# Kernel tuning notes

Hardware: AMD Instinct MI355X
Metric: run time of the kernel (lower is better)

## Reference

```python
import jax, jax.numpy as jnp
import numpy as np

CTX = 768   # ctx_len in the original module
C = 768     # n_embd
B = 16
T = 768
K_EPS = 1e-8


def setup_inputs() -> dict:
    key = jax.random.key(0)
    ks = jax.random.split(key, 10)
    scale = 1.0 / np.sqrt(C)
    x = jax.random.normal(ks[0], (B, T, C), jnp.float32)
    time_decay = jax.random.normal(ks[1], (C, 1), jnp.float32) * 0.1
    time_first = jnp.full((C, 1), np.log(0.3), jnp.float32)
    time_mix_k = jax.random.uniform(ks[2], (1, 1, C), jnp.float32)
    time_mix_v = jax.random.uniform(ks[3], (1, 1, C), jnp.float32)
    time_mix_r = jax.random.uniform(ks[4], (1, 1, C), jnp.float32)
    Wk = jax.random.normal(ks[5], (C, C), jnp.float32) * scale
    Wv = jax.random.normal(ks[6], (C, C), jnp.float32) * scale
    Wr = jax.random.normal(ks[7], (C, C), jnp.float32) * scale
    Wo = jax.random.normal(ks[8], (C, C), jnp.float32) * scale
    return {"x": x, "time_decay": time_decay, "time_first": time_first,
            "time_mix_k": time_mix_k, "time_mix_v": time_mix_v, "time_mix_r": time_mix_r,
            "Wk": Wk, "Wv": Wv, "Wr": Wr, "Wo": Wo}


def reference(x, time_decay, time_first, time_mix_k, time_mix_v, time_mix_r, Wk, Wv, Wr, Wo):
    Bb, Tt, Cc = x.shape
    # time_shift: xx[t] = x[t-1], xx[0] = 0
    xx = jnp.pad(x, ((0, 0), (1, 0), (0, 0)))[:, :Tt]
    xk = x * time_mix_k + xx * (1.0 - time_mix_k)
    xv = x * time_mix_v + xx * (1.0 - time_mix_v)
    xr = x * time_mix_r + xx * (1.0 - time_mix_r)
    # projections (nn.Linear, no bias: y = x @ W.T); k, v laid out [B, C, T]
    k = jnp.einsum('btc,oc->bot', xk, Wk)
    v = jnp.einsum('btc,oc->bot', xv, Wv)
    r = jnp.einsum('btc,oc->bto', xr, Wr)
    k = jnp.exp(jnp.minimum(k, 60.0))
    kv = k * v
    # decay kernel: time_w = cat([exp(time_decay)*time_curve, time_first]); w = exp(time_w)[:, -T:]
    curve = (jnp.arange(CTX - 1) - (CTX - 2)).astype(x.dtype)  # [-(CTX-2) .. 0]
    tw = jnp.concatenate([jnp.exp(time_decay) * curve[None, :], time_first], axis=-1)  # [C, CTX]
    w = jnp.exp(tw)[:, -Tt:]            # [C, T]
    kern = w[:, None, :]                # [C, 1, T] depthwise kernel

    def causal_conv(z):  # z: [B, C, T] -> [B, C, T], left-padded cross-correlation
        return jax.lax.conv_general_dilated(
            z, kern, window_strides=(1,), padding=[(Tt - 1, 0)],
            feature_group_count=Cc, dimension_numbers=('NCH', 'OIH', 'NCH'))

    wkv = causal_conv(kv)
    wk = causal_conv(k) + K_EPS
    rwkv = jax.nn.sigmoid(r) * jnp.transpose(wkv / wk, (0, 2, 1))  # [B, T, C]
    return jnp.einsum('btc,oc->bto', rwkv, Wo)
```

## Files before the change

kernel.cpp:

```cpp
#include <hip/hip_runtime.h>
#include <math.h>

#define Mq 12288
#define Nq 768
#define Kq 768
#define Tq 768
#define Bq 16
#define Cq 768
#define BK 64
#define BM 128

typedef __bf16 bf16x8 __attribute__((ext_vector_type(8)));
typedef __bf16 bf16x4 __attribute__((ext_vector_type(4)));
typedef __bf16 bf16x2 __attribute__((ext_vector_type(2)));
typedef float  floatx4 __attribute__((ext_vector_type(4)));

#define GLD_LDS16(g, l) __builtin_amdgcn_global_load_lds(                      \
    (const __attribute__((address_space(1))) unsigned int*)(g),                \
    (__attribute__((address_space(3))) unsigned int*)(l), 16, 0, 0)

__global__ __launch_bounds__(256)
void prep_kernel(const float* __restrict__ x,
                 const float* __restrict__ mk, const float* __restrict__ mv,
                 const float* __restrict__ mr,
                 const float* __restrict__ Wk, const float* __restrict__ Wv,
                 const float* __restrict__ Wr, const float* __restrict__ Wo,
                 __bf16* __restrict__ xk, __bf16* __restrict__ xv,
                 __bf16* __restrict__ xr, __bf16* __restrict__ wp)
{
    const int bid = blockIdx.x;
    if (bid < 9216) {
        const int i  = bid * 256 + threadIdx.x;
        const int c4 = i % (Cq / 4);
        const int m  = i / (Cq / 4);
        const int t  = m % Tq;
        const int c0 = c4 * 4;

        const float4 xc = *(const float4*)(x + (size_t)m * Cq + c0);
        float4 xp = make_float4(0.f, 0.f, 0.f, 0.f);
        if (t > 0) xp = *(const float4*)(x + (size_t)(m - 1) * Cq + c0);

        const float4 k4 = *(const float4*)(mk + c0);
        const float4 v4 = *(const float4*)(mv + c0);
        const float4 r4 = *(const float4*)(mr + c0);

        bf16x4 ok = { (__bf16)fmaf(k4.x, xc.x - xp.x, xp.x),
                      (__bf16)fmaf(k4.y, xc.y - xp.y, xp.y),
                      (__bf16)fmaf(k4.z, xc.z - xp.z, xp.z),
                      (__bf16)fmaf(k4.w, xc.w - xp.w, xp.w) };
        bf16x4 ov = { (__bf16)fmaf(v4.x, xc.x - xp.x, xp.x),
                      (__bf16)fmaf(v4.y, xc.y - xp.y, xp.y),
                      (__bf16)fmaf(v4.z, xc.z - xp.z, xp.z),
                      (__bf16)fmaf(v4.w, xc.w - xp.w, xp.w) };
        bf16x4 orr = { (__bf16)fmaf(r4.x, xc.x - xp.x, xp.x),
                       (__bf16)fmaf(r4.y, xc.y - xp.y, xp.y),
                       (__bf16)fmaf(r4.z, xc.z - xp.z, xp.z),
                       (__bf16)fmaf(r4.w, xc.w - xp.w, xp.w) };
        const size_t o = (size_t)m * Cq + c0;
        *(bf16x4*)(xk + o) = ok;
        *(bf16x4*)(xv + o) = ov;
        *(bf16x4*)(xr + o) = orr;
    } else {
        const int i   = (bid - 9216) * 256 + threadIdx.x;
        const int a   = i / 147456;
        const int off = (i - a * 147456) * 4;
        const float* s = (a == 0) ? Wk : (a == 1) ? Wv : (a == 2) ? Wr : Wo;
        const float4 v = *(const float4*)(s + off);
        bf16x4 r = { (__bf16)v.x, (__bf16)v.y, (__bf16)v.z, (__bf16)v.w };
        *(bf16x4*)(wp + (size_t)a * 589824 + off) = r;
    }
}

template<bool KVR>
__global__ __launch_bounds__(256, 3)
void mfma_gemm(const __bf16* __restrict__ A0, const __bf16* __restrict__ A1,
               const __bf16* __restrict__ A2,
               const __bf16* __restrict__ W,
               __bf16* __restrict__ OUTb, float* __restrict__ OUTf)
{
    __shared__ __bf16 As[BM * BK];
    __shared__ __bf16 Bs[128 * BK];

    const int STRIPS = KVR ? 18 : 6;

    const int i_    = blockIdx.x;
    const int xcd   = i_ & 7;
    const int j_    = i_ >> 3;
    const int strip = j_ % STRIPS;
    const int mt    = xcd * 12 + j_ / STRIPS;

    const int tid   = threadIdx.x;
    const int wave  = tid >> 6;
    const int lane  = tid & 63;
    const int m0    = mt * BM;
    const int matid = KVR ? strip / 6 : 0;
    const int n0    = KVR ? (strip % 6) * 128 : strip * 128;
    const int wn0   = strip * 128;

    const __bf16* A = KVR ? (matid == 0 ? A0 : matid == 1 ? A1 : A2) : A0;

    const int r8 = lane >> 3;
    const int sc = (lane & 7) ^ r8;
    const __bf16* gA[4];  __bf16* lA[4];
    const __bf16* gB[4];  __bf16* lB[4];
#pragma unroll
    for (int i = 0; i < 4; ++i) {
        const int row = (wave * 4 + i) * 8 + r8;
        gA[i] = A + (size_t)(m0 + row) * Kq + sc * 8;
        lA[i] = As + (wave * 4 + i) * 512;
        gB[i] = W + (size_t)(wn0 + row) * Kq + sc * 8;
        lB[i] = Bs + (wave * 4 + i) * 512;
    }

    const int wm   = wave & 1;
    const int wn   = wave >> 1;
    const int xRow = wm * 64 + (lane & 15);
    const int wRow = wn * 64 + (lane & 15);
    const int lk   = lane >> 4;

    floatx4 acc[4][4];
#pragma unroll
    for (int i = 0; i < 4; ++i)
#pragma unroll
        for (int j = 0; j < 4; ++j) acc[i][j] = (floatx4){0.f, 0.f, 0.f, 0.f};

    for (int kt = 0; kt < Kq / BK; ++kt) {
#pragma unroll
        for (int i = 0; i < 4; ++i) { GLD_LDS16(gA[i], lA[i]); gA[i] += BK; }
#pragma unroll
        for (int i = 0; i < 4; ++i) { GLD_LDS16(gB[i], lB[i]); gB[i] += BK; }
        __syncthreads();

#pragma unroll
        for (int kk = 0; kk < 2; ++kk) {
            bf16x8 wF[4], xF[4];
#pragma unroll
            for (int i = 0; i < 4; ++i) {
                const int r = wRow + i * 16;
                wF[i] = *(const bf16x8*)(Bs + r * BK +
                                         (((kk << 2) | lk) ^ (r & 7)) * 8);
            }
#pragma unroll
            for (int j = 0; j < 4; ++j) {
                const int r = xRow + j * 16;
                xF[j] = *(const bf16x8*)(As + r * BK +
                                         (((kk << 2) | lk) ^ (r & 7)) * 8);
            }
#pragma unroll
            for (int i = 0; i < 4; ++i)
#pragma unroll
                for (int j = 0; j < 4; ++j)
                    acc[i][j] = __builtin_amdgcn_mfma_f32_16x16x32_bf16(
                        wF[i], xF[j], acc[i][j], 0, 0, 0);
        }
        __syncthreads();
    }

#pragma unroll
    for (int j = 0; j < 4; ++j) {
        const int tok = m0 + wm * 64 + j * 16 + (lane & 15);
#pragma unroll
        for (int i = 0; i < 4; ++i) {
            const int ch = n0 + wn * 64 + i * 16 + (lane >> 4) * 4;
            if (KVR) {
                float v0 = acc[i][j][0], v1 = acc[i][j][1];
                float v2 = acc[i][j][2], v3 = acc[i][j][3];
                if (matid == 0) {
                    v0 = expf(fminf(v0, 60.f)); v1 = expf(fminf(v1, 60.f));
                    v2 = expf(fminf(v2, 60.f)); v3 = expf(fminf(v3, 60.f));
                } else if (matid == 2) {
                    v0 = __builtin_amdgcn_rcpf(1.f + expf(-v0));
                    v1 = __builtin_amdgcn_rcpf(1.f + expf(-v1));
                    v2 = __builtin_amdgcn_rcpf(1.f + expf(-v2));
                    v3 = __builtin_amdgcn_rcpf(1.f + expf(-v3));
                }
                bf16x4 o = { (__bf16)v0, (__bf16)v1, (__bf16)v2, (__bf16)v3 };
                *(bf16x4*)(OUTb + (size_t)matid * Mq * Nq +
                           (size_t)tok * Nq + ch) = o;
            } else {
                floatx4 o = acc[i][j];
                *(floatx4*)(OUTf + (size_t)tok * Nq + ch) = o;
            }
        }
    }
}

#define SEG 16
#define SLEN (Tq / SEG)

__global__ __launch_bounds__(1024)
void scan_kernel(const __bf16* __restrict__ kb, const __bf16* __restrict__ vb,
                 __bf16* rb,
                 const float* __restrict__ td, const float* __restrict__ tf)
{
    __shared__ float2 aS[SEG][64];
    __shared__ float2 bS[SEG][64];

    const int cx  = threadIdx.x;
    const int seg = threadIdx.y;
    const int c0  = blockIdx.x * 128 + cx * 2;
    const int b   = blockIdx.y;

    const float d0 = expf(td[c0]),     d1 = expf(td[c0 + 1]);
    const float w0 = expf(-d0),        w1 = expf(-d1);
    const float u0 = expf(tf[c0]),     u1 = expf(tf[c0 + 1]);

    const size_t base = ((size_t)b * Tq + seg * SLEN) * Cq + c0;

    float a0 = 0.f, a1 = 0.f, s0 = 0.f, s1 = 0.f;
#pragma unroll 4
    for (int t = 0; t < SLEN; ++t) {
        const size_t idx = base + (size_t)t * Cq;
        const bf16x2 k2 = *(const bf16x2*)(kb + idx);
        const bf16x2 v2 = *(const bf16x2*)(vb + idx);
        const float k0 = (float)k2[0], k1 = (float)k2[1];
        a0 = fmaf(w0, a0, k0 * (float)v2[0]);
        a1 = fmaf(w1, a1, k1 * (float)v2[1]);
        s0 = fmaf(w0, s0, k0);
        s1 = fmaf(w1, s1, k1);
    }
    aS[seg][cx] = make_float2(a0, a1);
    bS[seg][cx] = make_float2(s0, s1);
    __syncthreads();

    if (seg == 0) {
        const float W0 = expf(-d0 * (float)SLEN);
        const float W1 = expf(-d1 * (float)SLEN);
        float ia0 = 0.f, ia1 = 0.f, ib0 = 0.f, ib1 = 0.f;
#pragma unroll
        for (int s = 0; s < SEG; ++s) {
            const float2 ta = aS[s][cx];
            const float2 tb = bS[s][cx];
            aS[s][cx] = make_float2(ia0, ia1);
            bS[s][cx] = make_float2(ib0, ib1);
            ia0 = fmaf(W0, ia0, ta.x);  ia1 = fmaf(W1, ia1, ta.y);
            ib0 = fmaf(W0, ib0, tb.x);  ib1 = fmaf(W1, ib1, tb.y);
        }
    }
    __syncthreads();

    const float2 ain = aS[seg][cx];
    const float2 bin = bS[seg][cx];
    a0 = ain.x; a1 = ain.y; s0 = bin.x; s1 = bin.y;
#pragma unroll 2
    for (int t = 0; t < SLEN; ++t) {
        const size_t idx = base + (size_t)t * Cq;
        const bf16x2 k2 = *(const bf16x2*)(kb + idx);
        const bf16x2 v2 = *(const bf16x2*)(vb + idx);
        const bf16x2 r2 = *(const bf16x2*)(rb + idx);
        const float k0 = (float)k2[0], k1 = (float)k2[1];
        const float kv0 = k0 * (float)v2[0], kv1 = k1 * (float)v2[1];
        const float n0 = fmaf(u0, kv0, a0), n1 = fmaf(u1, kv1, a1);
        const float e0 = fmaf(u0, k0, s0) + 1e-8f;
        const float e1 = fmaf(u1, k1, s1) + 1e-8f;
        const float i0 = __builtin_amdgcn_rcpf(e0);
        const float i1 = __builtin_amdgcn_rcpf(e1);
        bf16x2 o = { (__bf16)((float)r2[0] * n0 * i0),
                     (__bf16)((float)r2[1] * n1 * i1) };
        *(bf16x2*)(rb + idx) = o;
        a0 = fmaf(w0, a0, kv0);  a1 = fmaf(w1, a1, kv1);
        s0 = fmaf(w0, s0, k0);   s1 = fmaf(w1, s1, k1);
    }
}

extern "C" void kernel_launch(void* const* d_in, const int* in_sizes, int n_in,
                              void* d_out, int out_size, void* d_ws, size_t ws_size,
                              hipStream_t stream)
{
    const float* x  = (const float*)d_in[0];
    const float* td = (const float*)d_in[1];
    const float* tf = (const float*)d_in[2];
    const float* mk = (const float*)d_in[3];
    const float* mv = (const float*)d_in[4];
    const float* mr = (const float*)d_in[5];
    const float* Wk = (const float*)d_in[6];
    const float* Wv = (const float*)d_in[7];
    const float* Wr = (const float*)d_in[8];
    const float* Wo = (const float*)d_in[9];

    const size_t MC = (size_t)Mq * Cq;

    __bf16* xk = (__bf16*)d_out;
    __bf16* xv = xk + MC;

    __bf16* xr   = (__bf16*)d_ws;
    __bf16* kbuf = xr + MC;
    __bf16* vbuf = kbuf + MC;
    __bf16* rbuf = vbuf + MC;
    __bf16* Wp   = rbuf + MC;
    __bf16* Wob  = Wp + 3 * 589824;

    prep_kernel<<<11520, 256, 0, stream>>>(x, mk, mv, mr, Wk, Wv, Wr, Wo,
                                           xk, xv, xr, Wp);

    mfma_gemm<true><<<18 * 96, 256, 0, stream>>>(
        xk, xv, xr, Wp, kbuf, nullptr);

    scan_kernel<<<dim3(Cq / 128, Bq), dim3(64, SEG), 0, stream>>>(
        kbuf, vbuf, rbuf, td, tf);

    mfma_gemm<false><<<6 * 96, 256, 0, stream>>>(
        rbuf, nullptr, nullptr, Wob, nullptr, (float*)d_out);
}
```

Before: 216.5 us.

## Fuse token-shift mixing into the KVR projection GEMM A-tile load

Removes the separate prep pass that wrote bf16 xk/xv/xr to memory. The KVR GEMM now loads fp32 x (current and previous row) directly, applies the time-mix, converts to bf16 and writes the A tile into LDS with regular stores. This saves the intermediate write and re-read of three activation tensors. The cost is that each of the six N-strips per matrix recomputes the mix and reads fp32 x twice, and the asynchronous global-to-LDS load for A is replaced by synchronous register loads with no overlap.

```diff
diff --git a/kernel.cpp b/kernel.cpp
--- a/kernel.cpp
+++ b/kernel.cpp
@@ -20,68 +20,30 @@
     (__attribute__((address_space(3))) unsigned int*)(l), 16, 0, 0)
 
 __global__ __launch_bounds__(256)
-void prep_kernel(const float* __restrict__ x,
-                 const float* __restrict__ mk, const float* __restrict__ mv,
-                 const float* __restrict__ mr,
-                 const float* __restrict__ Wk, const float* __restrict__ Wv,
-                 const float* __restrict__ Wr, const float* __restrict__ Wo,
-                 __bf16* __restrict__ xk, __bf16* __restrict__ xv,
-                 __bf16* __restrict__ xr, __bf16* __restrict__ wp)
-{
-    const int bid = blockIdx.x;
-    if (bid < 9216) {
-        const int i  = bid * 256 + threadIdx.x;
-        const int c4 = i % (Cq / 4);
-        const int m  = i / (Cq / 4);
-        const int t  = m % Tq;
-        const int c0 = c4 * 4;
-
-        const float4 xc = *(const float4*)(x + (size_t)m * Cq + c0);
-        float4 xp = make_float4(0.f, 0.f, 0.f, 0.f);
-        if (t > 0) xp = *(const float4*)(x + (size_t)(m - 1) * Cq + c0);
-
-        const float4 k4 = *(const float4*)(mk + c0);
-        const float4 v4 = *(const float4*)(mv + c0);
-        const float4 r4 = *(const float4*)(mr + c0);
-
-        bf16x4 ok = { (__bf16)fmaf(k4.x, xc.x - xp.x, xp.x),
-                      (__bf16)fmaf(k4.y, xc.y - xp.y, xp.y),
-                      (__bf16)fmaf(k4.z, xc.z - xp.z, xp.z),
-                      (__bf16)fmaf(k4.w, xc.w - xp.w, xp.w) };
-        bf16x4 ov = { (__bf16)fmaf(v4.x, xc.x - xp.x, xp.x),
-                      (__bf16)fmaf(v4.y, xc.y - xp.y, xp.y),
-                      (__bf16)fmaf(v4.z, xc.z - xp.z, xp.z),
-                      (__bf16)fmaf(v4.w, xc.w - xp.w, xp.w) };
-        bf16x4 orr = { (__bf16)fmaf(r4.x, xc.x - xp.x, xp.x),
-                       (__bf16)fmaf(r4.y, xc.y - xp.y, xp.y),
-                       (__bf16)fmaf(r4.z, xc.z - xp.z, xp.z),
-                       (__bf16)fmaf(r4.w, xc.w - xp.w, xp.w) };
-        const size_t o = (size_t)m * Cq + c0;
-        *(bf16x4*)(xk + o) = ok;
-        *(bf16x4*)(xv + o) = ov;
-        *(bf16x4*)(xr + o) = orr;
-    } else {
-        const int i   = (bid - 9216) * 256 + threadIdx.x;
-        const int a   = i / 147456;
-        const int off = (i - a * 147456) * 4;
-        const float* s = (a == 0) ? Wk : (a == 1) ? Wv : (a == 2) ? Wr : Wo;
-        const float4 v = *(const float4*)(s + off);
-        bf16x4 r = { (__bf16)v.x, (__bf16)v.y, (__bf16)v.z, (__bf16)v.w };
-        *(bf16x4*)(wp + (size_t)a * 589824 + off) = r;
-    }
-}
-
-template<bool KVR>
+void prep_w(const float* __restrict__ Wk, const float* __restrict__ Wv,
+            const float* __restrict__ Wr, const float* __restrict__ Wo,
+            __bf16* __restrict__ wp)
+{
+    const int i   = blockIdx.x * 256 + threadIdx.x;
+    const int a   = i / 147456;
+    const int off = (i - a * 147456) * 4;
+    const float* s = (a == 0) ? Wk : (a == 1) ? Wv : (a == 2) ? Wr : Wo;
+    const float4 v = *(const float4*)(s + off);
+    bf16x4 r = { (__bf16)v.x, (__bf16)v.y, (__bf16)v.z, (__bf16)v.w };
+    *(bf16x4*)(wp + (size_t)a * 589824 + off) = r;
+}
+
 __global__ __launch_bounds__(256, 3)
-void mfma_gemm(const __bf16* __restrict__ A0, const __bf16* __restrict__ A1,
-               const __bf16* __restrict__ A2,
-               const __bf16* __restrict__ W,
-               __bf16* __restrict__ OUTb, float* __restrict__ OUTf)
+void gemm_kvr_f(const float* __restrict__ X,
+                const float* __restrict__ mk, const float* __restrict__ mv,
+                const float* __restrict__ mr,
+                const __bf16* __restrict__ W,
+                __bf16* __restrict__ OUTb)
 {
     __shared__ __bf16 As[BM * BK];
     __shared__ __bf16 Bs[128 * BK];
 
-    const int STRIPS = KVR ? 18 : 6;
+    const int STRIPS = 18;
 
     const int i_    = blockIdx.x;
     const int xcd   = i_ & 7;
@@ -93,23 +55,30 @@
     const int wave  = tid >> 6;
     const int lane  = tid & 63;
     const int m0    = mt * BM;
-    const int matid = KVR ? strip / 6 : 0;
-    const int n0    = KVR ? (strip % 6) * 128 : strip * 128;
+    const int matid = strip / 6;
+    const int n0    = (strip % 6) * 128;
     const int wn0   = strip * 128;
 
-    const __bf16* A = KVR ? (matid == 0 ? A0 : matid == 1 ? A1 : A2) : A0;
+    const float* MIX = (matid == 0) ? mk : (matid == 1) ? mv : mr;
 
     const int r8 = lane >> 3;
     const int sc = (lane & 7) ^ r8;
-    const __bf16* gA[4];  __bf16* lA[4];
     const __bf16* gB[4];  __bf16* lB[4];
 #pragma unroll
     for (int i = 0; i < 4; ++i) {
         const int row = (wave * 4 + i) * 8 + r8;
-        gA[i] = A + (size_t)(m0 + row) * Kq + sc * 8;
-        lA[i] = As + (wave * 4 + i) * 512;
         gB[i] = W + (size_t)(wn0 + row) * Kq + sc * 8;
         lB[i] = Bs + (wave * 4 + i) * 512;
+    }
+
+    const float* gx[4];  bool zb[4];  __bf16* wA[4];
+#pragma unroll
+    for (int i = 0; i < 4; ++i) {
+        const int rowl = (wave * 4 + i) * 8 + r8;
+        const int grow = m0 + rowl;
+        gx[i] = X + (size_t)grow * Cq + sc * 8;
+        zb[i] = (grow % Tq) == 0;
+        wA[i] = As + rowl * 64 + (lane & 7) * 8;
     }
 
     const int wm   = wave & 1;
@@ -126,9 +95,32 @@
 
     for (int kt = 0; kt < Kq / BK; ++kt) {
 #pragma unroll
-        for (int i = 0; i < 4; ++i) { GLD_LDS16(gA[i], lA[i]); gA[i] += BK; }
-#pragma unroll
         for (int i = 0; i < 4; ++i) { GLD_LDS16(gB[i], lB[i]); gB[i] += BK; }
+
+        const float4 mA = *(const float4*)(MIX + kt * 64 + sc * 8);
+        const float4 mB = *(const float4*)(MIX + kt * 64 + sc * 8 + 4);
+#pragma unroll
+        for (int i = 0; i < 4; ++i) {
+            const float* xc = gx[i] + kt * 64;
+            const float4 c0 = *(const float4*)(xc);
+            const float4 c1 = *(const float4*)(xc + 4);
+            float4 p0 = make_float4(0.f, 0.f, 0.f, 0.f);
+            float4 p1 = make_float4(0.f, 0.f, 0.f, 0.f);
+            if (!zb[i]) {
+                p0 = *(const float4*)(xc - Cq);
+                p1 = *(const float4*)(xc - Cq + 4);
+            }
+            bf16x8 o;
+            o[0] = (__bf16)fmaf(mA.x, c0.x - p0.x, p0.x);
+            o[1] = (__bf16)fmaf(mA.y, c0.y - p0.y, p0.y);
+            o[2] = (__bf16)fmaf(mA.z, c0.z - p0.z, p0.z);
+            o[3] = (__bf16)fmaf(mA.w, c0.w - p0.w, p0.w);
+            o[4] = (__bf16)fmaf(mB.x, c1.x - p1.x, p1.x);
+            o[5] = (__bf16)fmaf(mB.y, c1.y - p1.y, p1.y);
+            o[6] = (__bf16)fmaf(mB.z, c1.z - p1.z, p1.z);
+            o[7] = (__bf16)fmaf(mB.w, c1.w - p1.w, p1.w);
+            *(bf16x8*)wA[i] = o;
+        }
         __syncthreads();
 
 #pragma unroll
@@ -162,25 +154,109 @@
 #pragma unroll
         for (int i = 0; i < 4; ++i) {
             const int ch = n0 + wn * 64 + i * 16 + (lane >> 4) * 4;
-            if (KVR) {
-                float v0 = acc[i][j][0], v1 = acc[i][j][1];
-                float v2 = acc[i][j][2], v3 = acc[i][j][3];
-                if (matid == 0) {
-                    v0 = expf(fminf(v0, 60.f)); v1 = expf(fminf(v1, 60.f));
-                    v2 = expf(fminf(v2, 60.f)); v3 = expf(fminf(v3, 60.f));
-                } else if (matid == 2) {
-                    v0 = __builtin_amdgcn_rcpf(1.f + expf(-v0));
-                    v1 = __builtin_amdgcn_rcpf(1.f + expf(-v1));
-                    v2 = __builtin_amdgcn_rcpf(1.f + expf(-v2));
-                    v3 = __builtin_amdgcn_rcpf(1.f + expf(-v3));
-                }
-                bf16x4 o = { (__bf16)v0, (__bf16)v1, (__bf16)v2, (__bf16)v3 };
-                *(bf16x4*)(OUTb + (size_t)matid * Mq * Nq +
-                           (size_t)tok * Nq + ch) = o;
-            } else {
-                floatx4 o = acc[i][j];
-                *(floatx4*)(OUTf + (size_t)tok * Nq + ch) = o;
-            }
+            float v0 = acc[i][j][0], v1 = acc[i][j][1];
+            float v2 = acc[i][j][2], v3 = acc[i][j][3];
+            if (matid == 0) {
+                v0 = expf(fminf(v0, 60.f)); v1 = expf(fminf(v1, 60.f));
+                v2 = expf(fminf(v2, 60.f)); v3 = expf(fminf(v3, 60.f));
+            } else if (matid == 2) {
+                v0 = __builtin_amdgcn_rcpf(1.f + expf(-v0));
+                v1 = __builtin_amdgcn_rcpf(1.f + expf(-v1));
+                v2 = __builtin_amdgcn_rcpf(1.f + expf(-v2));
+                v3 = __builtin_amdgcn_rcpf(1.f + expf(-v3));
+            }
+            bf16x4 o = { (__bf16)v0, (__bf16)v1, (__bf16)v2, (__bf16)v3 };
+            *(bf16x4*)(OUTb + (size_t)matid * Mq * Nq +
+                       (size_t)tok * Nq + ch) = o;
+        }
+    }
+}
+
+__global__ __launch_bounds__(256, 3)
+void gemm_o(const __bf16* __restrict__ A0, const __bf16* __restrict__ W,
+            float* __restrict__ OUTf)
+{
+    __shared__ __bf16 As[BM * BK];
+    __shared__ __bf16 Bs[128 * BK];
+
+    const int STRIPS = 6;
+    const int i_    = blockIdx.x;
+    const int xcd   = i_ & 7;
+    const int j_    = i_ >> 3;
+    const int strip = j_ % STRIPS;
+    const int mt    = xcd * 12 + j_ / STRIPS;
+
+    const int tid   = threadIdx.x;
+    const int wave  = tid >> 6;
+    const int lane  = tid & 63;
+    const int m0    = mt * BM;
+    const int n0    = strip * 128;
+
+    const int r8 = lane >> 3;
+    const int sc = (lane & 7) ^ r8;
+    const __bf16* gA[4];  __bf16* lA[4];
+    const __bf16* gB[4];  __bf16* lB[4];
+#pragma unroll
+    for (int i = 0; i < 4; ++i) {
+        const int row = (wave * 4 + i) * 8 + r8;
+        gA[i] = A0 + (size_t)(m0 + row) * Kq + sc * 8;
+        lA[i] = As + (wave * 4 + i) * 512;
+        gB[i] = W + (size_t)(n0 + row) * Kq + sc * 8;
+        lB[i] = Bs + (wave * 4 + i) * 512;
+    }
+
+    const int wm   = wave & 1;
+    const int wn   = wave >> 1;
+    const int xRow = wm * 64 + (lane & 15);
+    const int wRow = wn * 64 + (lane & 15);
+    const int lk   = lane >> 4;
+
+    floatx4 acc[4][4];
+#pragma unroll
+    for (int i = 0; i < 4; ++i)
+#pragma unroll
+        for (int j = 0; j < 4; ++j) acc[i][j] = (floatx4){0.f, 0.f, 0.f, 0.f};
+
+    for (int kt = 0; kt < Kq / BK; ++kt) {
+#pragma unroll
+        for (int i = 0; i < 4; ++i) { GLD_LDS16(gA[i], lA[i]); gA[i] += BK; }
+#pragma unroll
+        for (int i = 0; i < 4; ++i) { GLD_LDS16(gB[i], lB[i]); gB[i] += BK; }
+        __syncthreads();
+
+#pragma unroll
+        for (int kk = 0; kk < 2; ++kk) {
+            bf16x8 wF[4], xF[4];
+#pragma unroll
+            for (int i = 0; i < 4; ++i) {
+                const int r = wRow + i * 16;
+                wF[i] = *(const bf16x8*)(Bs + r * BK +
+                                         (((kk << 2) | lk) ^ (r & 7)) * 8);
+            }
+#pragma unroll
+            for (int j = 0; j < 4; ++j) {
+                const int r = xRow + j * 16;
+                xF[j] = *(const bf16x8*)(As + r * BK +
+                                         (((kk << 2) | lk) ^ (r & 7)) * 8);
+            }
+#pragma unroll
+            for (int i = 0; i < 4; ++i)
+#pragma unroll
+                for (int j = 0; j < 4; ++j)
+                    acc[i][j] = __builtin_amdgcn_mfma_f32_16x16x32_bf16(
+                        wF[i], xF[j], acc[i][j], 0, 0, 0);
+        }
+        __syncthreads();
+    }
+
+#pragma unroll
+    for (int j = 0; j < 4; ++j) {
+        const int tok = m0 + wm * 64 + j * 16 + (lane & 15);
+#pragma unroll
+        for (int i = 0; i < 4; ++i) {
+            const int ch = n0 + wn * 64 + i * 16 + (lane >> 4) * 4;
+            floatx4 o = acc[i][j];
+            *(floatx4*)(OUTf + (size_t)tok * Nq + ch) = o;
         }
     }
 }
@@ -280,25 +356,18 @@
 
     const size_t MC = (size_t)Mq * Cq;
 
-    __bf16* xk = (__bf16*)d_out;
-    __bf16* xv = xk + MC;
-
-    __bf16* xr   = (__bf16*)d_ws;
-    __bf16* kbuf = xr + MC;
+    __bf16* kbuf = (__bf16*)d_ws;
     __bf16* vbuf = kbuf + MC;
     __bf16* rbuf = vbuf + MC;
     __bf16* Wp   = rbuf + MC;
     __bf16* Wob  = Wp + 3 * 589824;
 
-    prep_kernel<<<11520, 256, 0, stream>>>(x, mk, mv, mr, Wk, Wv, Wr, Wo,
-                                           xk, xv, xr, Wp);
-
-    mfma_gemm<true><<<18 * 96, 256, 0, stream>>>(
-        xk, xv, xr, Wp, kbuf, nullptr);
+    prep_w<<<2304, 256, 0, stream>>>(Wk, Wv, Wr, Wo, Wp);
+
+    gemm_kvr_f<<<18 * 96, 256, 0, stream>>>(x, mk, mv, mr, Wp, kbuf);
 
     scan_kernel<<<dim3(Cq / 128, Bq), dim3(64, SEG), 0, stream>>>(
         kbuf, vbuf, rbuf, td, tf);
 
-    mfma_gemm<false><<<6 * 96, 256, 0, stream>>>(
-        rbuf, nullptr, nullptr, Wob, nullptr, (float*)d_out);
-}
+    gemm_o<<<6 * 96, 256, 0, stream>>>(rbuf, Wob, (float*)d_out);
+}
```

New measurement: 292.7 us. 35.2% more time.
